# Kernel tuning notes

Hardware: AMD Instinct MI355X
Metric: run time of the kernel (lower is better)

The kernel has to match this reference:

```python
import jax, jax.numpy as jnp
import numpy as np

N, E, NI, G = 100000, 50000, 2000000, 256
F_IN, H, HOUT, L = 92, 35, 64, 3
NEG = 0.2  # leaky_relu negative_slope (PyG default)


def _seg_softmax(scores, seg, num_seg):
    # PyG softmax grouped by segment id, with +1e-16 in the denominator
    m = jax.ops.segment_max(scores, seg, num_segments=num_seg)
    m = jnp.where(jnp.isfinite(m), m, 0.0)
    ex = jnp.exp(scores - m[seg])
    s = jax.ops.segment_sum(ex, seg, num_segments=num_seg)
    return ex / (s[seg] + 1e-16)


def setup_inputs() -> dict:
    key = jax.random.key(0)
    ks = jax.random.split(key, 10)
    return {
        "x": jax.random.normal(ks[0], (N, F_IN), jnp.float32),
        "hyperedge_attr": jax.random.normal(ks[1], (E, H), jnp.float32),
        "node_idx": jax.random.randint(ks[2], (NI,), 0, N, jnp.int32),
        "edge_idx": jax.random.randint(ks[3], (NI,), 0, E, jnp.int32),
        "batch": jnp.sort(jax.random.randint(ks[4], (N,), 0, G, jnp.int32)),
        "embed_W": jax.random.normal(ks[5], (F_IN, H), jnp.float32) * 0.1,
        "embed_b": jnp.zeros((H,), jnp.float32),
        "lin_W": jax.random.normal(ks[6], (L, H, H), jnp.float32) * 0.17,
        "att": jax.random.normal(ks[7], (L, 2 * H), jnp.float32) * 0.1,
        "conv_b": jnp.zeros((L, H), jnp.float32),
        "proj_W": jax.random.normal(ks[8], (H, HOUT), jnp.float32) * 0.17,
        "proj_b": jnp.zeros((HOUT,), jnp.float32),
        "out_W": jax.random.normal(ks[9], (HOUT, 1), jnp.float32) * 0.12,
        "out_b": jnp.zeros((1,), jnp.float32),
    }


def _hconv(x, he_attr, node_idx, edge_idx, W, att, b):
    # PyG HypergraphConv(use_attention=True, heads=1, attention_mode='node')
    xl = x @ W            # [N, H]  lin (bias=False)
    el = he_attr @ W      # [E, H]  same lin on hyperedge_attr
    s_n = xl @ att[:H]    # [N]  node half of att vector
    s_e = el @ att[H:]    # [E]  edge half of att vector
    alpha = jax.nn.leaky_relu(s_n[node_idx] + s_e[edge_idx], NEG)  # [NI]
    alpha = _seg_softmax(alpha, edge_idx, E)  # softmax over nodes within each hyperedge
    ones = jnp.ones_like(alpha)
    D = jax.ops.segment_sum(ones, node_idx, num_segments=N)   # node degree (hyperedge_weight=1)
    Dinv = jnp.where(D > 0, 1.0 / D, 0.0)
    B = jax.ops.segment_sum(ones, edge_idx, num_segments=E)   # hyperedge size
    Binv = jnp.where(B > 0, 1.0 / B, 0.0)
    # pass 1: node -> hyperedge, message = B_e * alpha * x_v
    m1 = (Binv[edge_idx] * alpha)[:, None] * xl[node_idx]      # [NI, H]
    e_out = jax.ops.segment_sum(m1, edge_idx, num_segments=E)  # [E, H]
    # pass 2: hyperedge -> node, message = D_v * alpha * e_out
    m2 = (Dinv[node_idx] * alpha)[:, None] * e_out[edge_idx]   # [NI, H]
    return jax.ops.segment_sum(m2, node_idx, num_segments=N) + b


def reference(x, hyperedge_attr, node_idx, edge_idx, batch, embed_W, embed_b,
              lin_W, att, conv_b, proj_W, proj_b, out_W, out_b):
    h = x @ embed_W + embed_b                                  # [N, 35]
    for l in range(L):
        h = _hconv(h, hyperedge_attr, node_idx, edge_idx, lin_W[l], att[l], conv_b[l])
    # scatter-mean graph pooling
    s = jax.ops.segment_sum(h, batch, num_segments=G)          # [G, 35]
    cnt = jax.ops.segment_sum(jnp.ones((h.shape[0],), h.dtype), batch, num_segments=G)
    pooled = s / jnp.maximum(cnt, 1.0)[:, None]
    z = jax.nn.softplus(pooled @ proj_W + proj_b)              # [G, 64]
    return z @ out_W + out_b                                   # [G, 1]
```

## Files before the change

kernel.cpp:

```cpp
#include <hip/hip_runtime.h>
#include <hip/hip_bf16.h>
#include <limits.h>
#include <math.h>

#define F_IN 92
#define H 35
#define HP 36
#define HOUT 64
#define NL 3
#define NEG_SLOPE 0.2f
#define NSLICE 8
#define SCH 2048

typedef int iv4 __attribute__((ext_vector_type(4)));


__global__ void embed_kernel(const float* __restrict__ x, const float* __restrict__ W,
                             const float* __restrict__ b, float* __restrict__ h, int N) {
    __shared__ float sW[F_IN * H];
    for (int t = threadIdx.x; t < F_IN * H; t += blockDim.x) sW[t] = W[t];
    __syncthreads();
    int total = N * HP;
    int stride = gridDim.x * blockDim.x;
    for (int t = blockIdx.x * blockDim.x + threadIdx.x; t < total; t += stride) {
        int n = t / HP, j = t - n * HP;
        if (j < H) {
            const float* xr = x + (long)n * F_IN;
            float acc = b[j];
#pragma unroll 4
            for (int k = 0; k < F_IN; ++k) acc += xr[k] * sW[k * H + j];
            h[t] = acc;
        } else {
            h[t] = 0.f;
        }
    }
}

__global__ void lin_kernel(const float* __restrict__ in, const float* __restrict__ W,
                           float* __restrict__ out, int R) {
    __shared__ float sW[H * H];
    for (int t = threadIdx.x; t < H * H; t += blockDim.x) sW[t] = W[t];
    __syncthreads();
    int total = R * HP;
    int stride = gridDim.x * blockDim.x;
    for (int t = blockIdx.x * blockDim.x + threadIdx.x; t < total; t += stride) {
        int r = t / HP, j = t - r * HP;
        if (j < H) {
            const float* ir = in + (long)r * HP;
            float acc = 0.f;
#pragma unroll
            for (int k = 0; k < H; ++k) acc += ir[k] * sW[k * H + j];
            out[t] = acc;
        } else {
            out[t] = 0.f;
        }
    }
}

__global__ void rowdot_kernel(const float* __restrict__ in, const float* __restrict__ vec,
                              float* __restrict__ s, int R, int stride_out) {
    __shared__ float sA[H];
    for (int t = threadIdx.x; t < H; t += blockDim.x) sA[t] = vec[t];
    __syncthreads();
    int stride = gridDim.x * blockDim.x;
    for (int r = blockIdx.x * blockDim.x + threadIdx.x; r < R; r += stride) {
        const float* xr = in + (long)r * HP;
        float acc = 0.f;
#pragma unroll
        for (int k = 0; k < H; ++k) acc += xr[k] * sA[k];
        s[(long)r * stride_out] = acc;
    }
}

__global__ void rowdot_he_kernel(const float* __restrict__ in, const float* __restrict__ vec,
                                 float* __restrict__ s, int R, int stride_out) {
    __shared__ float sA[H];
    for (int t = threadIdx.x; t < H; t += blockDim.x) sA[t] = vec[t];
    __syncthreads();
    int stride = gridDim.x * blockDim.x;
    for (int r = blockIdx.x * blockDim.x + threadIdx.x; r < R; r += stride) {
        const float* xr = in + (long)r * H;
        float acc = 0.f;
#pragma unroll
        for (int k = 0; k < H; ++k) acc += xr[k] * sA[k];
        s[(long)r * stride_out] = acc;
    }
}

__global__ void wfold_kernel(const float* __restrict__ W, const float* __restrict__ a,
                             float* __restrict__ w2) {
    int k = threadIdx.x;
    if (k < H) {
        float acc = 0.f;
#pragma unroll
        for (int j = 0; j < H; ++j) acc += W[k * H + j] * a[j];
        w2[k] = acc;
    }
}


__global__ void count_sliced_kernel(const int* __restrict__ ni, const int* __restrict__ ei,
                                    int* __restrict__ ncnt, int* __restrict__ ecnt,
                                    int ninc, int wN, int wE) {
    int s = blockIdx.x & (NSLICE - 1);
    int loN = s * wN, hiN = loN + wN;
    int loE = s * wE, hiE = loE + wE;
    int nblk = gridDim.x >> 3;
    int bid = blockIdx.x >> 3;
    int nvec = ninc >> 2;
    int stride = nblk * blockDim.x;
    for (int q = bid * blockDim.x + threadIdx.x; q < nvec; q += stride) {
        iv4 v4 = __builtin_nontemporal_load((const iv4*)ni + q);
        iv4 e4 = __builtin_nontemporal_load((const iv4*)ei + q);
#pragma unroll
        for (int u = 0; u < 4; ++u) {
            int e = e4[u], v = v4[u];
            if (e >= loE && e < hiE) atomicAdd(&ecnt[e], 1);
            if (v >= loN && v < hiN) atomicAdd(&ncnt[v], 1);
        }
    }
    if (bid == 0) {
        for (int i = (nvec << 2) + threadIdx.x; i < ninc; i += blockDim.x) {
            int v = ni[i], e = ei[i];
            if (e >= loE && e < hiE) atomicAdd(&ecnt[e], 1);
            if (v >= loN && v < hiN) atomicAdd(&ncnt[v], 1);
        }
    }
}

__device__ __forceinline__ int wave_sum_i(int s) {
#pragma unroll
    for (int off = 32; off; off >>= 1) s += __shfl_xor(s, off);
    return s;
}

__global__ void bsum2_kernel(const int* __restrict__ cnt0, int nb0, int n0,
                             const int* __restrict__ cnt1, int n1,
                             int* __restrict__ bsums) {
    int b = blockIdx.x;
    const int* c; int n; int base;
    if (b < nb0) { c = cnt0; n = n0; base = b * SCH; }
    else         { c = cnt1; n = n1; base = (b - nb0) * SCH; }
    int t = threadIdx.x;
    int hi = base + SCH; if (hi > n) hi = n;
    int s = 0;
    for (int i = base + t; i < hi; i += 256) s += c[i];
    s = wave_sum_i(s);
    __shared__ int ws[4];
    if ((t & 63) == 0) ws[t >> 6] = s;
    __syncthreads();
    if (t == 0) bsums[b] = ws[0] + ws[1] + ws[2] + ws[3];
}

__global__ void scan_bsums_kernel(int* __restrict__ bsums, int nb0, int nb1) {
    int t = threadIdx.x;
    if (t == 0) {
        int acc = 0;
        for (int i = 0; i < nb0; ++i) { int v = bsums[i]; bsums[i] = acc; acc += v; }
    } else if (t == 1) {
        int acc = 0;
        for (int i = nb0; i < nb0 + nb1; ++i) { int v = bsums[i]; bsums[i] = acc; acc += v; }
    }
}

__global__ void scan_write2_kernel(const int* __restrict__ cnt0, int* __restrict__ ptr0,
                                   int* __restrict__ cur0, int nb0, int n0,
                                   const int* __restrict__ cnt1, int* __restrict__ ptr1,
                                   int* __restrict__ cur1, int n1,
                                   const int* __restrict__ bsums, int ninc) {
    int b = blockIdx.x;
    const int* c; int* p; int* u; int n; int base;
    if (b < nb0) { c = cnt0; p = ptr0; u = cur0; n = n0; base = b * SCH; }
    else         { c = cnt1; p = ptr1; u = cur1; n = n1; base = (b - nb0) * SCH; }
    int off = bsums[b];
    int t = threadIdx.x;
    int lo = base + t * 8;
    int vals[8];
    int s = 0;
#pragma unroll
    for (int k = 0; k < 8; ++k) {
        int i = lo + k;
        int v = (i < n) ? c[i] : 0;
        vals[k] = s;
        s += v;
    }
    __shared__ int lds[256];
    lds[t] = s;
    __syncthreads();
    for (int o2 = 1; o2 < 256; o2 <<= 1) {
        int v = (t >= o2) ? lds[t - o2] : 0;
        __syncthreads();
        lds[t] += v;
        __syncthreads();
    }
    int tbase = off + ((t == 0) ? 0 : lds[t - 1]);
#pragma unroll
    for (int k = 0; k < 8; ++k) {
        int i = lo + k;
        if (i < n) { int val = tbase + vals[k]; p[i] = val; u[i] = val; }
    }
    if (b == 0 && t == 0) { ptr0[n0] = ninc; ptr1[n1] = ninc; }
}

__global__ void csr_fill_sliced_kernel(const int* __restrict__ ni, const int* __restrict__ ei,
                                       int* __restrict__ ecur, int* __restrict__ ncur,
                                       int* __restrict__ enode, int* __restrict__ nedge,
                                       int ninc, int wN, int wE) {
    int s = blockIdx.x & (NSLICE - 1);
    int loN = s * wN, hiN = loN + wN;
    int loE = s * wE, hiE = loE + wE;
    int nblk = gridDim.x >> 3;
    int bid = blockIdx.x >> 3;
    int nvec = ninc >> 2;
    int stride = nblk * blockDim.x;
    for (int q = bid * blockDim.x + threadIdx.x; q < nvec; q += stride) {
        iv4 v4 = __builtin_nontemporal_load((const iv4*)ni + q);
        iv4 e4 = __builtin_nontemporal_load((const iv4*)ei + q);
#pragma unroll
        for (int u = 0; u < 4; ++u) {
            int e = e4[u], v = v4[u];
            if (e >= loE && e < hiE) {
                int p = atomicAdd(&ecur[e], 1);
                enode[p] = v;
            }
            if (v >= loN && v < hiN) {
                int p = atomicAdd(&ncur[v], 1);
                nedge[p] = e;
            }
        }
    }
    if (bid == 0) {
        for (int i = (nvec << 2) + threadIdx.x; i < ninc; i += blockDim.x) {
            int v = ni[i], e = ei[i];
            if (e >= loE && e < hiE) { int p = atomicAdd(&ecur[e], 1); enode[p] = v; }
            if (v >= loN && v < hiN) { int p = atomicAdd(&ncur[v], 1); nedge[p] = e; }
        }
    }
}


__device__ __forceinline__ float wave_max(float m) {
#pragma unroll
    for (int off = 32; off; off >>= 1) m = fmaxf(m, __shfl_xor(m, off));
    return m;
}
__device__ __forceinline__ float wave_sum(float s) {
#pragma unroll
    for (int off = 32; off; off >>= 1) s += __shfl_xor(s, off);
    return s;
}

__device__ __forceinline__ void grouped_gather(const float* __restrict__ src,
                                               const float* shA, const int* shV,
                                               int cnt, int g, int l, float4& acc) {
    if (g < 7) {
        for (int k = g; k < cnt; k += 7) {
            float ak = shA[k];
            int vk = shV[k];
            float4 xv = ((const float4*)(src + (size_t)vk * HP))[l];
            acc.x += ak * xv.x; acc.y += ak * xv.y;
            acc.z += ak * xv.z; acc.w += ak * xv.w;
        }
    }
}

__device__ __forceinline__ void group_reduce(float4& acc, int lane, int l) {
#pragma unroll
    for (int gg = 1; gg < 7; ++gg) {
        int src = l + 9 * gg;
        float ox = __shfl(acc.x, src);
        float oy = __shfl(acc.y, src);
        float oz = __shfl(acc.z, src);
        float ow = __shfl(acc.w, src);
        if (lane < 9) { acc.x += ox; acc.y += oy; acc.z += oz; acc.w += ow; }
    }
}

__global__ void edge_pass_kernel(const int* __restrict__ eptr, const int* __restrict__ enode,
                                 const float* __restrict__ s_n, float* __restrict__ epack,
                                 const float* __restrict__ xl,
                                 float* __restrict__ e_out, int E) {
    __shared__ float shA[4][64];
    __shared__ int   shV[4][64];
    int lane = threadIdx.x & 63;
    int ws = threadIdx.x >> 6;
    int g = lane / 9, l = lane - g * 9;
    int wid = (blockIdx.x * blockDim.x + threadIdx.x) >> 6;
    int nw = (gridDim.x * blockDim.x) >> 6;
    for (int e = wid; e < E; e += nw) {
        int lo = eptr[e], hi = eptr[e + 1];
        int deg = hi - lo;
        float se = epack[4 * (long)e];
        float binv = deg > 0 ? 1.f / (float)deg : 0.f;
        float4 acc = {0.f, 0.f, 0.f, 0.f};
        float mm, rec;
        if (deg <= 64) {
            int v = 0; float sc = -INFINITY;
            if (lane < deg) {
                v = enode[lo + lane];
                sc = s_n[v] + se;
                sc = sc >= 0.f ? sc : NEG_SLOPE * sc;
            }
            float m = wave_max(sc);
            mm = (m == -INFINITY) ? 0.f : m;
            float ex = (lane < deg) ? expf(sc - mm) : 0.f;
            float s = wave_sum(ex);
            rec = 1.f / (s + 1e-16f);
            shA[ws][lane] = ex * rec * binv;
            shV[ws][lane] = v;
            grouped_gather(xl, shA[ws], shV[ws], deg, g, l, acc);
        } else {
            float m = -INFINITY;
            for (int k = lo + lane; k < hi; k += 64) {
                float sc = s_n[enode[k]] + se;
                sc = sc >= 0.f ? sc : NEG_SLOPE * sc;
                m = fmaxf(m, sc);
            }
            m = wave_max(m);
            mm = (m == -INFINITY) ? 0.f : m;
            float s = 0.f;
            for (int k = lo + lane; k < hi; k += 64) {
                float sc = s_n[enode[k]] + se;
                sc = sc >= 0.f ? sc : NEG_SLOPE * sc;
                s += expf(sc - mm);
            }
            s = wave_sum(s);
            rec = 1.f / (s + 1e-16f);
            float cb = rec * binv;
            for (int base = lo; base < hi; base += 64) {
                int v = 0; float a = 0.f;
                if (base + lane < hi) {
                    v = enode[base + lane];
                    float sc = s_n[v] + se;
                    sc = sc >= 0.f ? sc : NEG_SLOPE * sc;
                    a = expf(sc - mm) * cb;
                }
                shA[ws][lane] = a;
                shV[ws][lane] = v;
                int cn = hi - base; if (cn > 64) cn = 64;
                grouped_gather(xl, shA[ws], shV[ws], cn, g, l, acc);
            }
        }
        group_reduce(acc, lane, l);
        if (lane < 9) ((float4*)(e_out + (size_t)e * HP))[lane] = acc;
        if (lane == 0) { epack[4 * (long)e + 1] = mm; epack[4 * (long)e + 2] = rec; }
    }
}

__global__ void node_pass_kernel(const int* __restrict__ nptr, const int* __restrict__ nedge,
                                 const float* __restrict__ s_n, const float* __restrict__ epack,
                                 const float* __restrict__ e_out, const float* __restrict__ bias,
                                 float* __restrict__ hout, int N) {
    __shared__ float shA[4][64];
    __shared__ int   shE[4][64];
    __shared__ float sb[HP];
    if (threadIdx.x < HP) sb[threadIdx.x] = (threadIdx.x < H) ? bias[threadIdx.x] : 0.f;
    __syncthreads();
    int lane = threadIdx.x & 63;
    int ws = threadIdx.x >> 6;
    int g = lane / 9, l = lane - g * 9;
    int wid = (blockIdx.x * blockDim.x + threadIdx.x) >> 6;
    int nw = (gridDim.x * blockDim.x) >> 6;
    for (int v = wid; v < N; v += nw) {
        int lo = nptr[v], hi = nptr[v + 1];
        int deg = hi - lo;
        float dinv = deg > 0 ? 1.f / (float)deg : 0.f;
        float sn = s_n[v];
        float4 acc = {0.f, 0.f, 0.f, 0.f};
        if (deg <= 64) {
            int e = 0; float a = 0.f;
            if (lane < deg) {
                e = nedge[lo + lane];
                float4 p = ((const float4*)epack)[e];
                float sc = sn + p.x;
                sc = sc >= 0.f ? sc : NEG_SLOPE * sc;
                a = expf(sc - p.y) * p.z;
            }
            shA[ws][lane] = a;
            shE[ws][lane] = e;
            grouped_gather(e_out, shA[ws], shE[ws], deg, g, l, acc);
        } else {
            for (int base = lo; base < hi; base += 64) {
                int e = 0; float a = 0.f;
                if (base + lane < hi) {
                    e = nedge[base + lane];
                    float4 p = ((const float4*)epack)[e];
                    float sc = sn + p.x;
                    sc = sc >= 0.f ? sc : NEG_SLOPE * sc;
                    a = expf(sc - p.y) * p.z;
                }
                shA[ws][lane] = a;
                shE[ws][lane] = e;
                int cn = hi - base; if (cn > 64) cn = 64;
                grouped_gather(e_out, shA[ws], shE[ws], cn, g, l, acc);
            }
        }
        group_reduce(acc, lane, l);
        if (lane < 9) {
            float4 bb = ((const float4*)sb)[lane];
            float4 r;
            r.x = dinv * acc.x + bb.x;
            r.y = dinv * acc.y + bb.y;
            r.z = dinv * acc.z + bb.z;
            r.w = dinv * acc.w + bb.w;
            ((float4*)(hout + (size_t)v * HP))[lane] = r;
        }
    }
}

__global__ void pool_head_kernel(const float* __restrict__ h, const int* __restrict__ batch,
                                 int N, const float* __restrict__ pW, const float* __restrict__ pb,
                                 const float* __restrict__ oW, const float* __restrict__ ob,
                                 float* __restrict__ out) {
    int g = blockIdx.x;
    int t = threadIdx.x;
    __shared__ int bounds[2];
    __shared__ float partial[7][H];
    __shared__ float pooled[H];
    if (t == 0) {
        int lo = 0, hi = N;
        while (lo < hi) { int mid = (lo + hi) >> 1; if (batch[mid] < g) lo = mid + 1; else hi = mid; }
        bounds[0] = lo;
        int lo2 = lo, hi2 = N;
        while (lo2 < hi2) { int mid = (lo2 + hi2) >> 1; if (batch[mid] < g + 1) lo2 = mid + 1; else hi2 = mid; }
        bounds[1] = lo2;
    }
    __syncthreads();
    int rlo = bounds[0], rhi = bounds[1];
    int cntg = rhi - rlo;
    int gg = t / H;
    int j = t - gg * H;
    if (gg < 7) {
        float acc = 0.f;
        for (int r = rlo + gg; r < rhi; r += 7) acc += h[(long)r * HP + j];
        partial[gg][j] = acc;
    }
    __syncthreads();
    if (t < H) {
        float s = 0.f;
#pragma unroll
        for (int k = 0; k < 7; ++k) s += partial[k][t];
        pooled[t] = s / fmaxf((float)cntg, 1.f);
    }
    __syncthreads();
    if (t < HOUT) {
        float acc = pb[t];
#pragma unroll
        for (int k = 0; k < H; ++k) acc += pooled[k] * pW[k * HOUT + t];
        float z = fmaxf(acc, 0.f) + log1pf(expf(-fabsf(acc)));
        float pr = z * oW[t];
#pragma unroll
        for (int off = 32; off; off >>= 1) pr += __shfl_down(pr, off);
        if (t == 0) out[g] = pr + ob[0];
    }
}

static inline int grid_for(long n, int block = 256, long cap = 2048) {
    long b = (n + block - 1) / block;
    if (b > cap) b = cap;
    if (b < 1) b = 1;
    return (int)b;
}

extern "C" void kernel_launch(void* const* d_in, const int* in_sizes, int n_in,
                              void* d_out, int out_size, void* d_ws, size_t ws_size,
                              hipStream_t stream) {
    const float* x       = (const float*)d_in[0];
    const float* he      = (const float*)d_in[1];
    const int*   ni      = (const int*)d_in[2];
    const int*   ei      = (const int*)d_in[3];
    const int*   batch   = (const int*)d_in[4];
    const float* embed_W = (const float*)d_in[5];
    const float* embed_b = (const float*)d_in[6];
    const float* lin_W   = (const float*)d_in[7];
    const float* att     = (const float*)d_in[8];
    const float* conv_b  = (const float*)d_in[9];
    const float* proj_W  = (const float*)d_in[10];
    const float* proj_b  = (const float*)d_in[11];
    const float* out_W   = (const float*)d_in[12];
    const float* out_b   = (const float*)d_in[13];
    float* out = (float*)d_out;

    const int N    = in_sizes[0] / F_IN;
    const int E    = in_sizes[1] / H;
    const int NINC = in_sizes[2];
    const int G    = out_size;

    char* w = (char*)d_ws;
    auto alloc = [&](size_t bytes) {
        char* p = w;
        w += (bytes + 255) & ~(size_t)255;
        return p;
    };
    float* h     = (float*)alloc((size_t)N * HP * 4);
    float* xl    = (float*)alloc((size_t)N * HP * 4);
    float* e_out = (float*)alloc((size_t)E * HP * 4);
    float* s_n   = (float*)alloc((size_t)N * 4);
    float* epack = (float*)alloc((size_t)E * 16);
    float* w2    = (float*)alloc((size_t)H * 4);
    int*   ecnt  = (int*)alloc((size_t)E * 4);
    int*   eptr  = (int*)alloc((size_t)(E + 1) * 4);
    int*   ecur  = (int*)alloc((size_t)E * 4);
    int*   ncnt  = (int*)alloc((size_t)N * 4);
    int*   nptr  = (int*)alloc((size_t)(N + 1) * 4);
    int*   ncur  = (int*)alloc((size_t)N * 4);
    int*   enode = (int*)alloc((size_t)NINC * 4);
    int*   nedge = (int*)alloc((size_t)NINC * 4);
    int*   bsums = (int*)alloc((size_t)256 * 4);

    const int BLK = 256;
    int gNH  = grid_for((long)N * HP);
    int gN   = grid_for(N);
    int gE   = grid_for(E);
    int wN   = (N + NSLICE - 1) / NSLICE;
    int wE   = (E + NSLICE - 1) / NSLICE;
    int nbE  = (E + SCH - 1) / SCH;
    int nbN  = (N + SCH - 1) / SCH;

    (void)hipMemsetAsync(ncnt, 0, (size_t)N * 4, stream);
    (void)hipMemsetAsync(ecnt, 0, (size_t)E * 4, stream);
    count_sliced_kernel<<<2048, BLK, 0, stream>>>(ni, ei, ncnt, ecnt, NINC, wN, wE);
    bsum2_kernel<<<nbE + nbN, 256, 0, stream>>>(ecnt, nbE, E, ncnt, N, bsums);
    scan_bsums_kernel<<<1, 64, 0, stream>>>(bsums, nbE, nbN);
    scan_write2_kernel<<<nbE + nbN, 256, 0, stream>>>(ecnt, eptr, ecur, nbE, E,
                                                      ncnt, nptr, ncur, N, bsums, NINC);
    csr_fill_sliced_kernel<<<2048, BLK, 0, stream>>>(ni, ei, ecur, ncur, enode, nedge,
                                                     NINC, wN, wE);

    embed_kernel<<<gNH, BLK, 0, stream>>>(x, embed_W, embed_b, h, N);

    int gEdge = (E + 3) / 4;
    int gNode = (N + 3) / 4;
    for (int l = 0; l < NL; ++l) {
        const float* W  = lin_W + (size_t)l * H * H;
        const float* at = att + (size_t)l * 2 * H;
        const float* b  = conv_b + (size_t)l * H;

        lin_kernel<<<gNH, BLK, 0, stream>>>(h, W, xl, N);
        rowdot_kernel<<<gN, BLK, 0, stream>>>(xl, at, s_n, N, 1);
        wfold_kernel<<<1, 64, 0, stream>>>(W, at + H, w2);
        rowdot_he_kernel<<<gE, BLK, 0, stream>>>(he, w2, epack, E, 4);

        edge_pass_kernel<<<gEdge, BLK, 0, stream>>>(eptr, enode, s_n, epack, xl, e_out, E);
        node_pass_kernel<<<gNode, BLK, 0, stream>>>(nptr, nedge, s_n, epack, e_out, b, h, N);
    }

    pool_head_kernel<<<G, BLK, 0, stream>>>(h, batch, N, proj_W, proj_b, out_W, out_b, out);
}
```

Before: 1.014 ms.

## Store gathered node features and hyperedge outputs in fp16

Measured after the change: 940.3 us. 1.08x faster.

```diff
diff --git a/kernel.cpp b/kernel.cpp
--- a/kernel.cpp
+++ b/kernel.cpp
@@ -1,11 +1,13 @@
 #include <hip/hip_runtime.h>
 #include <hip/hip_bf16.h>
+#include <hip/hip_fp16.h>
 #include <limits.h>
 #include <math.h>
 
 #define F_IN 92
 #define H 35
 #define HP 36
+#define HP2 36
 #define HOUT 64
 #define NL 3
 #define NEG_SLOPE 0.2f
@@ -36,23 +38,23 @@
     }
 }
 
-__global__ void lin_kernel(const float* __restrict__ in, const float* __restrict__ W,
-                           float* __restrict__ out, int R) {
+__global__ void lin_h_kernel(const float* __restrict__ in, const float* __restrict__ W,
+                             __half* __restrict__ out, int R) {
     __shared__ float sW[H * H];
     for (int t = threadIdx.x; t < H * H; t += blockDim.x) sW[t] = W[t];
     __syncthreads();
-    int total = R * HP;
+    int total = R * HP2;
     int stride = gridDim.x * blockDim.x;
     for (int t = blockIdx.x * blockDim.x + threadIdx.x; t < total; t += stride) {
-        int r = t / HP, j = t - r * HP;
+        int r = t / HP2, j = t - r * HP2;
         if (j < H) {
             const float* ir = in + (long)r * HP;
             float acc = 0.f;
 #pragma unroll
             for (int k = 0; k < H; ++k) acc += ir[k] * sW[k * H + j];
-            out[t] = acc;
+            out[t] = __float2half(acc);
         } else {
-            out[t] = 0.f;
+            out[t] = __float2half(0.f);
         }
     }
 }
@@ -87,14 +89,20 @@
     }
 }
 
-__global__ void wfold_kernel(const float* __restrict__ W, const float* __restrict__ a,
-                             float* __restrict__ w2) {
+__global__ void wfold2_kernel(const float* __restrict__ W, const float* __restrict__ an,
+                              const float* __restrict__ ae,
+                              float* __restrict__ w1, float* __restrict__ w2) {
     int k = threadIdx.x;
     if (k < H) {
-        float acc = 0.f;
-#pragma unroll
-        for (int j = 0; j < H; ++j) acc += W[k * H + j] * a[j];
-        w2[k] = acc;
+        float acc1 = 0.f, acc2 = 0.f;
+#pragma unroll
+        for (int j = 0; j < H; ++j) {
+            float wkj = W[k * H + j];
+            acc1 += wkj * an[j];
+            acc2 += wkj * ae[j];
+        }
+        w1[k] = acc1;
+        w2[k] = acc2;
     }
 }
 
@@ -250,16 +258,20 @@
     return s;
 }
 
-__device__ __forceinline__ void grouped_gather(const float* __restrict__ src,
-                                               const float* shA, const int* shV,
-                                               int cnt, int g, int l, float4& acc) {
+__device__ __forceinline__ void grouped_gather_h(const __half* __restrict__ src,
+                                                 const float* shA, const int* shV,
+                                                 int cnt, int g, int l, float4& acc) {
     if (g < 7) {
         for (int k = g; k < cnt; k += 7) {
             float ak = shA[k];
             int vk = shV[k];
-            float4 xv = ((const float4*)(src + (size_t)vk * HP))[l];
-            acc.x += ak * xv.x; acc.y += ak * xv.y;
-            acc.z += ak * xv.z; acc.w += ak * xv.w;
+            uint2 raw = ((const uint2*)(src + (size_t)vk * HP2))[l];
+            __half2 h01 = *reinterpret_cast<const __half2*>(&raw.x);
+            __half2 h23 = *reinterpret_cast<const __half2*>(&raw.y);
+            float2 f01 = __half22float2(h01);
+            float2 f23 = __half22float2(h23);
+            acc.x += ak * f01.x; acc.y += ak * f01.y;
+            acc.z += ak * f23.x; acc.w += ak * f23.y;
         }
     }
 }
@@ -278,8 +290,8 @@
 
 __global__ void edge_pass_kernel(const int* __restrict__ eptr, const int* __restrict__ enode,
                                  const float* __restrict__ s_n, float* __restrict__ epack,
-                                 const float* __restrict__ xl,
-                                 float* __restrict__ e_out, int E) {
+                                 const __half* __restrict__ xl_h,
+                                 __half* __restrict__ e_out_h, int E) {
     __shared__ float shA[4][64];
     __shared__ int   shV[4][64];
     int lane = threadIdx.x & 63;
@@ -308,7 +320,7 @@
             rec = 1.f / (s + 1e-16f);
             shA[ws][lane] = ex * rec * binv;
             shV[ws][lane] = v;
-            grouped_gather(xl, shA[ws], shV[ws], deg, g, l, acc);
+            grouped_gather_h(xl_h, shA[ws], shV[ws], deg, g, l, acc);
         } else {
             float m = -INFINITY;
             for (int k = lo + lane; k < hi; k += 64) {
@@ -338,18 +350,25 @@
                 shA[ws][lane] = a;
                 shV[ws][lane] = v;
                 int cn = hi - base; if (cn > 64) cn = 64;
-                grouped_gather(xl, shA[ws], shV[ws], cn, g, l, acc);
+                grouped_gather_h(xl_h, shA[ws], shV[ws], cn, g, l, acc);
             }
         }
         group_reduce(acc, lane, l);
-        if (lane < 9) ((float4*)(e_out + (size_t)e * HP))[lane] = acc;
+        if (lane < 9) {
+            __half2 p0 = __floats2half2_rn(acc.x, acc.y);
+            __half2 p1 = __floats2half2_rn(acc.z, acc.w);
+            uint2 wv;
+            wv.x = *reinterpret_cast<unsigned*>(&p0);
+            wv.y = *reinterpret_cast<unsigned*>(&p1);
+            ((uint2*)(e_out_h + (size_t)e * HP2))[lane] = wv;
+        }
         if (lane == 0) { epack[4 * (long)e + 1] = mm; epack[4 * (long)e + 2] = rec; }
     }
 }
 
 __global__ void node_pass_kernel(const int* __restrict__ nptr, const int* __restrict__ nedge,
                                  const float* __restrict__ s_n, const float* __restrict__ epack,
-                                 const float* __restrict__ e_out, const float* __restrict__ bias,
+                                 const __half* __restrict__ e_out_h, const float* __restrict__ bias,
                                  float* __restrict__ hout, int N) {
     __shared__ float shA[4][64];
     __shared__ int   shE[4][64];
@@ -378,7 +397,7 @@
             }
             shA[ws][lane] = a;
             shE[ws][lane] = e;
-            grouped_gather(e_out, shA[ws], shE[ws], deg, g, l, acc);
+            grouped_gather_h(e_out_h, shA[ws], shE[ws], deg, g, l, acc);
         } else {
             for (int base = lo; base < hi; base += 64) {
                 int e = 0; float a = 0.f;
@@ -392,7 +411,7 @@
                 shA[ws][lane] = a;
                 shE[ws][lane] = e;
                 int cn = hi - base; if (cn > 64) cn = 64;
-                grouped_gather(e_out, shA[ws], shE[ws], cn, g, l, acc);
+                grouped_gather_h(e_out_h, shA[ws], shE[ws], cn, g, l, acc);
             }
         }
         group_reduce(acc, lane, l);
@@ -492,21 +511,22 @@
         w += (bytes + 255) & ~(size_t)255;
         return p;
     };
-    float* h     = (float*)alloc((size_t)N * HP * 4);
-    float* xl    = (float*)alloc((size_t)N * HP * 4);
-    float* e_out = (float*)alloc((size_t)E * HP * 4);
-    float* s_n   = (float*)alloc((size_t)N * 4);
-    float* epack = (float*)alloc((size_t)E * 16);
-    float* w2    = (float*)alloc((size_t)H * 4);
-    int*   ecnt  = (int*)alloc((size_t)E * 4);
-    int*   eptr  = (int*)alloc((size_t)(E + 1) * 4);
-    int*   ecur  = (int*)alloc((size_t)E * 4);
-    int*   ncnt  = (int*)alloc((size_t)N * 4);
-    int*   nptr  = (int*)alloc((size_t)(N + 1) * 4);
-    int*   ncur  = (int*)alloc((size_t)N * 4);
-    int*   enode = (int*)alloc((size_t)NINC * 4);
-    int*   nedge = (int*)alloc((size_t)NINC * 4);
-    int*   bsums = (int*)alloc((size_t)256 * 4);
+    float*  h       = (float*)alloc((size_t)N * HP * 4);
+    __half* xl_h    = (__half*)alloc((size_t)N * HP2 * 2);
+    __half* e_out_h = (__half*)alloc((size_t)E * HP2 * 2);
+    float*  s_n     = (float*)alloc((size_t)N * 4);
+    float*  epack   = (float*)alloc((size_t)E * 16);
+    float*  w1      = (float*)alloc((size_t)H * 4);
+    float*  w2      = (float*)alloc((size_t)H * 4);
+    int*    ecnt    = (int*)alloc((size_t)E * 4);
+    int*    eptr    = (int*)alloc((size_t)(E + 1) * 4);
+    int*    ecur    = (int*)alloc((size_t)E * 4);
+    int*    ncnt    = (int*)alloc((size_t)N * 4);
+    int*    nptr    = (int*)alloc((size_t)(N + 1) * 4);
+    int*    ncur    = (int*)alloc((size_t)N * 4);
+    int*    enode   = (int*)alloc((size_t)NINC * 4);
+    int*    nedge   = (int*)alloc((size_t)NINC * 4);
+    int*    bsums   = (int*)alloc((size_t)256 * 4);
 
     const int BLK = 256;
     int gNH  = grid_for((long)N * HP);
@@ -536,13 +556,13 @@
         const float* at = att + (size_t)l * 2 * H;
         const float* b  = conv_b + (size_t)l * H;
 
-        lin_kernel<<<gNH, BLK, 0, stream>>>(h, W, xl, N);
-        rowdot_kernel<<<gN, BLK, 0, stream>>>(xl, at, s_n, N, 1);
-        wfold_kernel<<<1, 64, 0, stream>>>(W, at + H, w2);
+        lin_h_kernel<<<gNH, BLK, 0, stream>>>(h, W, xl_h, N);
+        wfold2_kernel<<<1, 64, 0, stream>>>(W, at, at + H, w1, w2);
+        rowdot_kernel<<<gN, BLK, 0, stream>>>(h, w1, s_n, N, 1);
         rowdot_he_kernel<<<gE, BLK, 0, stream>>>(he, w2, epack, E, 4);
 
-        edge_pass_kernel<<<gEdge, BLK, 0, stream>>>(eptr, enode, s_n, epack, xl, e_out, E);
-        node_pass_kernel<<<gNode, BLK, 0, stream>>>(nptr, nedge, s_n, epack, e_out, b, h, N);
+        edge_pass_kernel<<<gEdge, BLK, 0, stream>>>(eptr, enode, s_n, epack, xl_h, e_out_h, E);
+        node_pass_kernel<<<gNode, BLK, 0, stream>>>(nptr, nedge, s_n, epack, e_out_h, b, h, N);
     }
 
     pool_head_kernel<<<G, BLK, 0, stream>>>(h, batch, N, proj_W, proj_b, out_W, out_b, out);
```
